# Optimization experiments

Measured on AMD Instinct MI355X. Metric: run time of the kernel, lower is better.

## Reference

```python
import jax, jax.numpy as jnp
import numpy as np


def _conv(x, w, b, pad):
    y = jax.lax.conv_general_dilated(
        x, w, window_strides=(1, 1), padding=[(pad, pad), (pad, pad)],
        dimension_numbers=('NCHW', 'OIHW', 'NCHW'))
    return y + b[None, :, None, None]


def _grid_sample(img, gxn, gyn):
    # img [N,C,H,W]; gxn,gyn [N,H,W] normalized coords.
    # Matches torch grid_sample(mode='bilinear', padding_mode='zeros', align_corners=False).
    N, C, H, W = img.shape
    ix = ((gxn + 1.0) * W - 1.0) * 0.5
    iy = ((gyn + 1.0) * H - 1.0) * 0.5
    ix0 = jnp.floor(ix); iy0 = jnp.floor(iy)
    ix1 = ix0 + 1.0; iy1 = iy0 + 1.0
    wx1 = ix - ix0; wy1 = iy - iy0
    wx0 = 1.0 - wx1; wy0 = 1.0 - wy1
    bidx = jnp.arange(N)[:, None, None]

    def gather(yy, xx):
        valid = (xx >= 0) & (xx < W) & (yy >= 0) & (yy < H)
        xc = jnp.clip(xx, 0, W - 1).astype(jnp.int32)
        yc = jnp.clip(yy, 0, H - 1).astype(jnp.int32)
        v = img[bidx, :, yc, xc]  # [N,H,W,C]
        return jnp.where(valid[..., None], v, jnp.zeros((), img.dtype))

    out = (gather(iy0, ix0) * (wy0 * wx0)[..., None]
           + gather(iy0, ix1) * (wy0 * wx1)[..., None]
           + gather(iy1, ix0) * (wy1 * wx0)[..., None]
           + gather(iy1, ix1) * (wy1 * wx1)[..., None])
    return jnp.transpose(out, (0, 3, 1, 2))  # [N,C,H,W]


def reference(inputs, state, i2h_w, i2h_b, i2f_w, i2f_b, h2f_w, h2f_b,
              flows_w, flows_b, wrap_w, wrap_b):
    B, T, Cin, H, W = inputs.shape
    hid = state.shape[1]
    L = flows_w.shape[0] // 2

    # input-to-hidden for all timesteps at once (as in the torch code)
    i2h = _conv(inputs.reshape(B * T, Cin, H, W), i2h_w, i2h_b, 1)
    i2h = i2h.reshape(B, T, 3 * hid, H, W)
    r_i, u_i, n_i = jnp.split(i2h, 3, axis=2)

    gx, gy = jnp.meshgrid(jnp.arange(W, dtype=inputs.dtype),
                          jnp.arange(H, dtype=inputs.dtype))  # each [H,W]

    def step(h, xs):
        x_t, r_t, u_t, n_t = xs
        f = jnp.tanh(_conv(x_t, i2f_w, i2f_b, 2) + _conv(h, h2f_w, h2f_b, 2))
        flows = _conv(f, flows_w, flows_b, 2).reshape(B, L, 2, H, W)
        # vgrid = grid + (-flow), then normalize by 2*v/size - 1
        vx = gx[None, None] - flows[:, :, 0]
        vy = gy[None, None] - flows[:, :, 1]
        gxn = 2.0 * vx / W - 1.0
        gyn = 2.0 * vy / H - 1.0
        img = jnp.broadcast_to(h[:, None], (B, L, hid, H, W)).reshape(B * L, hid, H, W)
        warped = _grid_sample(img, gxn.reshape(B * L, H, W), gyn.reshape(B * L, H, W))
        warped = warped.reshape(B, L * hid, H, W)
        h2h = _conv(warped, wrap_w, wrap_b, 0)
        r_h, u_h, n_h = jnp.split(h2h, 3, axis=1)
        r = jax.nn.sigmoid(r_t + r_h)
        u = jax.nn.sigmoid(u_t + u_h)
        n = jax.nn.sigmoid(n_t + r * n_h)  # note: sigmoid, faithful to source
        h_new = (1.0 - u) * n + u * h
        return h_new, h_new

    xs = (jnp.swapaxes(inputs, 0, 1),
          jnp.swapaxes(r_i, 0, 1),
          jnp.swapaxes(u_i, 0, 1),
          jnp.swapaxes(n_i, 0, 1))
    h_last, outs = jax.lax.scan(step, state, xs)
    outputs = jnp.swapaxes(outs, 0, 1)  # [B,T,hid,H,W]
    return outputs, h_last


def setup_inputs() -> dict:
    key = jax.random.key(0)
    ks = jax.random.split(key, 8)
    B, T, Cin, H, W = 4, 10, 8, 96, 96
    hid, L = 64, 13

    def w(k, shape):
        fan_in = int(np.prod(shape[1:]))
        return jax.random.normal(k, shape, jnp.float32) * (1.0 / np.sqrt(fan_in))

    return {
        'inputs': jax.random.normal(ks[0], (B, T, Cin, H, W), jnp.float32),
        'state': jnp.zeros((B, hid, H, W), jnp.float32),
        'i2h_w': w(ks[1], (3 * hid, Cin, 3, 3)), 'i2h_b': jnp.zeros((3 * hid,), jnp.float32),
        'i2f_w': w(ks[2], (32, Cin, 5, 5)), 'i2f_b': jnp.zeros((32,), jnp.float32),
        'h2f_w': w(ks[3], (32, hid, 5, 5)), 'h2f_b': jnp.zeros((32,), jnp.float32),
        'flows_w': w(ks[4], (2 * L, 32, 5, 5)), 'flows_b': jnp.zeros((2 * L,), jnp.float32),
        'wrap_w': w(ks[5], (3 * hid, hid * L, 1, 1)), 'wrap_b': jnp.zeros((3 * hid,), jnp.float32),
    }
```

## Files before the change

kernel.cpp:

```cpp
#include <hip/hip_runtime.h>
#include <math.h>

#define HW 9216

typedef __attribute__((ext_vector_type(8))) short short8;
typedef __attribute__((ext_vector_type(4))) short short4v;
typedef __attribute__((ext_vector_type(4))) float float4v;

__device__ __forceinline__ float sigmoidf_(float x) { return 1.0f / (1.0f + expf(-x)); }

__device__ __forceinline__ short bf16rne(float f) {
  unsigned u = __builtin_bit_cast(unsigned, f);
  unsigned r = (u + 0x7FFFu + ((u >> 16) & 1u)) >> 16;
  return (short)r;
}
__device__ __forceinline__ float bf2f(short s) {
  return __builtin_bit_cast(float, ((unsigned)(unsigned short)s) << 16);
}

__global__ __launch_bounds__(256) void k_wconv(const float* __restrict__ w,
                                               short* __restrict__ o)
{
  int i = blockIdx.x * 256 + threadIdx.x;
  if (i >= 192 * 832) return;
  int n = i / 832, k = i % 832;
  int l = k >> 6, c = k & 63;
  o[((size_t)l * 192 + n) * 64 + c] = bf16rne(w[i]);
}

__global__ __launch_bounds__(256) void k_pack(
    const float* __restrict__ wh, const float* __restrict__ wi,
    const float* __restrict__ flw, const float* __restrict__ wih,
    short* __restrict__ whK, short* __restrict__ wiK, short* __restrict__ flK,
    short* __restrict__ i2hK)
{
  int i = blockIdx.x * 256 + threadIdx.x;
  if (i < 51200) {
    int t = i / 2048, rem = i % 2048;
    int o = rem / 64, c = rem % 64;
    whK[i] = bf16rne(wh[((size_t)(o * 64 + c)) * 25 + t]);
  } else if (i < 58368) {
    int j = i - 51200;
    int g = j / 1024, rem = j % 1024;
    int o = rem / 32, k = rem % 32;
    int q = k / 8, ch = k % 8;
    int tap = g * 4 + q;
    wiK[j] = (tap < 25) ? bf16rne(wi[((size_t)(o * 8 + ch)) * 25 + tap]) : (short)0;
  } else if (i < 83968) {
    int j = i - 58368;
    int t = j / 1024, rem = j % 1024;
    int o = rem / 32, c = rem % 32;
    flK[j] = (o < 26) ? bf16rne(flw[((size_t)(o * 32 + c)) * 25 + t]) : (short)0;
  } else {
    int j = i - 83968;
    int g = j / 6144, rem = j % 6144;
    int n = rem / 32, k = rem % 32;
    int q = k / 8, ch = k % 8;
    int tap = g * 4 + q;
    i2hK[j] = (tap < 9) ? bf16rne(wih[((size_t)(n * 8 + ch)) * 9 + tap]) : (short)0;
  }
}

__global__ __launch_bounds__(256) void k_h2bf(const float* __restrict__ st,
                                              short* __restrict__ hbf)
{
  const int tid = threadIdx.x;
  const int pp = tid & 63, cg = tid >> 6;
  const int b = blockIdx.y;
  const int p = blockIdx.x * 64 + pp;
  short s[16];
  #pragma unroll
  for (int k = 0; k < 16; ++k)
    s[k] = bf16rne(st[((size_t)b * 64 + cg * 16 + k) * HW + p]);
  short* dst = hbf + ((size_t)b * HW + p) * 64 + cg * 16;
  *(short8*)dst = *(short8*)&s[0];
  *(short8*)(dst + 8) = *(short8*)&s[8];
}

__global__ __launch_bounds__(256) void k_x2bf(const float* __restrict__ inp,
                                              short* __restrict__ xbf)
{
  const int p  = blockIdx.x * 256 + threadIdx.x;
  const int bt = blockIdx.y;
  short s[8];
  #pragma unroll
  for (int ci = 0; ci < 8; ++ci)
    s[ci] = bf16rne(inp[((size_t)bt * 8 + ci) * HW + p]);
  *(short8*)(xbf + ((size_t)bt * HW + p) * 8) = *(short8*)s;
}

__global__ __launch_bounds__(256) void k_i2h(
    const short* __restrict__ xbf, int t_off,
    const short* __restrict__ wK, const float* __restrict__ bias,
    short* __restrict__ out)
{
  __shared__ __align__(16) short lds_o[192 * 136];
  const int tid  = threadIdx.x;
  const int lane = tid & 63;
  const int w    = tid >> 6;
  const int ml = lane & 15, qd = lane >> 4;
  const int zz = blockIdx.y;
  const int t = (zz >> 2) + t_off, b = zz & 3;
  const int pw0 = blockIdx.x * 128 + w * 32;
  const short* xb = xbf + ((size_t)(b * 10 + t)) * HW * 8;

  short8 afr[2][3];
  #pragma unroll
  for (int s = 0; s < 2; ++s) {
    int px0 = pw0 + s * 16;
    int y0 = px0 / 96, xc0 = px0 % 96;
    #pragma unroll
    for (int g = 0; g < 3; ++g) {
      int tap = g * 4 + qd;
      int dy = tap / 3 - 1;
      int dx = tap % 3 - 1;
      int yy = y0 + dy, xx = xc0 + ml + dx;
      bool v = (tap < 9) && (yy >= 0) && (yy < 96) && (xx >= 0) && (xx < 96);
      short8 a = {};
      if (v) a = *(const short8*)(xb + (size_t)(px0 + ml + dy * 96 + dx) * 8);
      afr[s][g] = a;
    }
  }

  float4v acc[2][12];
  #pragma unroll
  for (int s = 0; s < 2; ++s)
    #pragma unroll
    for (int j = 0; j < 12; ++j)
      #pragma unroll
      for (int r = 0; r < 4; ++r) acc[s][j][r] = 0.0f;

  #pragma unroll
  for (int j = 0; j < 12; ++j) {
    #pragma unroll
    for (int g = 0; g < 3; ++g) {
      short8 bf = *(const short8*)(wK + ((size_t)(g * 192 + j * 16 + ml)) * 32 + qd * 8);
      acc[0][j] = __builtin_amdgcn_mfma_f32_16x16x32_bf16(afr[0][g], bf, acc[0][j], 0, 0, 0);
      acc[1][j] = __builtin_amdgcn_mfma_f32_16x16x32_bf16(afr[1][g], bf, acc[1][j], 0, 0, 0);
    }
  }

  #pragma unroll
  for (int j = 0; j < 12; ++j) {
    float bv = bias[j * 16 + ml];
    #pragma unroll
    for (int s = 0; s < 2; ++s) {
      short4v o4;
      #pragma unroll
      for (int r = 0; r < 4; ++r) o4[r] = bf16rne(acc[s][j][r] + bv);
      *(short4v*)(lds_o + (j * 16 + ml) * 136 + w * 32 + s * 16 + qd * 4) = o4;
    }
  }
  __syncthreads();
  const int pblk = blockIdx.x * 128;
  #pragma unroll
  for (int k = 0; k < 12; ++k) {
    int r = (tid >> 4) + k * 16;
    short8 vvv = *(short8*)(lds_o + r * 136 + (tid & 15) * 8);
    *(short8*)(out + ((size_t)(zz * 192 + r)) * HW + pblk + (tid & 15) * 8) = vvv;
  }
}

__global__ __launch_bounds__(256) void k_f(
    const short* __restrict__ xbf, int t,
    const short* __restrict__ hbf,
    const short* __restrict__ whK,
    const short* __restrict__ wiK,
    const float* __restrict__ bi, const float* __restrict__ bh,
    short* __restrict__ fbf)
{
  const int tid = threadIdx.x;
  const int lane = tid & 63;
  const int w = tid >> 6;
  const int ml = lane & 15, qd = lane >> 4;
  const int b = blockIdx.y;
  const int px0 = blockIdx.x * 64 + w * 16;
  const int y0 = px0 / 96, xc0 = px0 % 96;
  const int xcol = xc0 + ml;
  const int px = px0 + ml;
  const short* hb = hbf + (size_t)b * HW * 64;
  const short* xb = xbf + ((size_t)(b * 10 + t)) * HW * 8;

  float4v acc0 = {0.f, 0.f, 0.f, 0.f};
  float4v acc1 = {0.f, 0.f, 0.f, 0.f};

  #pragma unroll
  for (int ky = 0; ky < 5; ++ky) {
    int yy = y0 + ky - 2;
    if (yy < 0 || yy >= 96) continue;
    #pragma unroll
    for (int kx = 0; kx < 5; ++kx) {
      int xx = xcol + kx - 2;
      bool cv = (xx >= 0) && (xx < 96);
      int off = (ky - 2) * 96 + (kx - 2);
      const short* ap = hb + (size_t)(px + off) * 64 + qd * 8;
      short8 a0 = {}, a1 = {};
      if (cv) { a0 = *(const short8*)ap; a1 = *(const short8*)(ap + 32); }
      int tap = ky * 5 + kx;
      const short* bp = whK + ((size_t)tap * 32 + ml) * 64 + qd * 8;
      short8 b00 = *(const short8*)bp;
      short8 b01 = *(const short8*)(bp + 32);
      short8 b10 = *(const short8*)(bp + 16 * 64);
      short8 b11 = *(const short8*)(bp + 16 * 64 + 32);
      acc0 = __builtin_amdgcn_mfma_f32_16x16x32_bf16(a0, b00, acc0, 0, 0, 0);
      acc0 = __builtin_amdgcn_mfma_f32_16x16x32_bf16(a1, b01, acc0, 0, 0, 0);
      acc1 = __builtin_amdgcn_mfma_f32_16x16x32_bf16(a0, b10, acc1, 0, 0, 0);
      acc1 = __builtin_amdgcn_mfma_f32_16x16x32_bf16(a1, b11, acc1, 0, 0, 0);
    }
  }

  #pragma unroll
  for (int g = 0; g < 7; ++g) {
    int tap = g * 4 + qd;
    int dy = tap / 5 - 2;
    int dx = tap - (dy + 2) * 5 - 2;
    int yy = y0 + dy, xx = xcol + dx;
    bool v = (tap < 25) && (yy >= 0) && (yy < 96) && (xx >= 0) && (xx < 96);
    short8 a = {};
    if (v) a = *(const short8*)(xb + (size_t)(px + dy * 96 + dx) * 8);
    const short* bp = wiK + ((size_t)g * 32 + ml) * 32 + qd * 8;
    short8 b0 = *(const short8*)bp;
    short8 b1 = *(const short8*)(bp + 16 * 32);
    acc0 = __builtin_amdgcn_mfma_f32_16x16x32_bf16(a, b0, acc0, 0, 0, 0);
    acc1 = __builtin_amdgcn_mfma_f32_16x16x32_bf16(a, b1, acc1, 0, 0, 0);
  }

  short* fo = fbf + (size_t)b * HW * 32;
  #pragma unroll
  for (int i = 0; i < 2; ++i) {
    int o = i * 16 + ml;
    float bias = bi[o] + bh[o];
    float4v a = i ? acc1 : acc0;
    #pragma unroll
    for (int r = 0; r < 4; ++r) {
      int p2 = px0 + qd * 4 + r;
      fo[(size_t)p2 * 32 + o] = bf16rne(tanhf(a[r] + bias));
    }
  }
}

__global__ __launch_bounds__(256) void k_flows(
    const short* __restrict__ fbf,
    const short* __restrict__ flK,
    const float* __restrict__ bias,
    float* __restrict__ fls)
{
  const int tid = threadIdx.x;
  const int lane = tid & 63;
  const int w = tid >> 6;
  const int ml = lane & 15, qd = lane >> 4;
  const int b = blockIdx.y;
  const int px0 = blockIdx.x * 64 + w * 16;
  const int y0 = px0 / 96, xc0 = px0 % 96;
  const int xcol = xc0 + ml;
  const int px = px0 + ml;
  const short* fb = fbf + (size_t)b * HW * 32;

  float4v acc0 = {0.f, 0.f, 0.f, 0.f};
  float4v acc1 = {0.f, 0.f, 0.f, 0.f};

  #pragma unroll
  for (int ky = 0; ky < 5; ++ky) {
    int yy = y0 + ky - 2;
    if (yy < 0 || yy >= 96) continue;
    #pragma unroll
    for (int kx = 0; kx < 5; ++kx) {
      int xx = xcol + kx - 2;
      bool cv = (xx >= 0) && (xx < 96);
      int off = (ky - 2) * 96 + (kx - 2);
      short8 a = {};
      if (cv) a = *(const short8*)(fb + (size_t)(px + off) * 32 + qd * 8);
      int tap = ky * 5 + kx;
      const short* bp = flK + ((size_t)tap * 32 + ml) * 32 + qd * 8;
      short8 b0 = *(const short8*)bp;
      short8 b1 = *(const short8*)(bp + 16 * 32);
      acc0 = __builtin_amdgcn_mfma_f32_16x16x32_bf16(a, b0, acc0, 0, 0, 0);
      acc1 = __builtin_amdgcn_mfma_f32_16x16x32_bf16(a, b1, acc1, 0, 0, 0);
    }
  }

  float* fo = fls + (size_t)b * 26 * HW;
  #pragma unroll
  for (int i = 0; i < 2; ++i) {
    int o = i * 16 + ml;
    if (o < 26) {
      float bv = bias[o];
      float4v a = i ? acc1 : acc0;
      #pragma unroll
      for (int r = 0; r < 4; ++r)
        fo[(size_t)o * HW + px0 + qd * 4 + r] = a[r] + bv;
    }
  }
}

__global__ __launch_bounds__(256, 3) void k_fused(
    const float* __restrict__ fls,
    const float* __restrict__ hbase, long long hstr,
    const short* __restrict__ hbf_in,
    const short* __restrict__ i2h,
    const short* __restrict__ wbf,
    const float* __restrict__ wb,
    float* __restrict__ outb, long long ostr,
    short* __restrict__ hbf_out,
    float* __restrict__ lastb)
{
  __shared__ __align__(16) char smem_raw[49920];
  short* lds_w = (short*)smem_raw;
  short* lds_v = lds_w + 192 * 72;
  float* lds_f = (float*)(smem_raw + 36864);
  float* lds_h = (float*)smem_raw;
  short* hpack = (short*)smem_raw;

  const int tid = threadIdx.x;
  const int pp  = tid & 63;
  const int cg  = tid >> 6;
  const int ii  = blockIdx.x;
  const int xcd = ii & 7;
  const int b   = xcd >> 1;
  const int tile = ((ii >> 3) << 1) | (xcd & 1);
  const int p   = tile * 64 + pp;
  const int ypix = p / 96, xpix = p % 96;
  const float* hb  = hbase + (size_t)b * hstr;
  const short* hvp = hbf_in + ((size_t)b * HW) * 64 + cg * 16;
  const float* flb = fls + (size_t)b * 26 * HW;
  const int ml = pp & 15;
  const int qd = pp >> 4;

  #pragma unroll
  for (int it = 0; it < 7; ++it) {
    int idx = it * 256 + tid;
    if (idx < 1664) {
      int c = idx >> 6, pp2 = idx & 63;
      lds_f[pp2 * 26 + c] = flb[(size_t)c * HW + tile * 64 + pp2];
    }
  }

  float4v acc[3][4];
  #pragma unroll
  for (int i = 0; i < 3; ++i)
    #pragma unroll
    for (int j = 0; j < 4; ++j)
      #pragma unroll
      for (int r = 0; r < 4; ++r) acc[i][j][r] = 0.0f;

  int   o_[4];
  float wt_[4];
  short8 u_[4][2];
  short8 wreg[6];
  short vv[16];

  auto comp_offs = [&](int l) {
    float fx = lds_f[pp * 26 + 2 * l];
    float fy = lds_f[pp * 26 + 2 * l + 1];
    float vx = (float)xpix - fx;
    float vy = (float)ypix - fy;
    float gxn = 2.0f * vx / 96.0f - 1.0f;
    float gyn = 2.0f * vy / 96.0f - 1.0f;
    float ix = ((gxn + 1.0f) * 96.0f - 1.0f) * 0.5f;
    float iy = ((gyn + 1.0f) * 96.0f - 1.0f) * 0.5f;
    float x0f = floorf(ix), y0f = floorf(iy);
    float wx1 = ix - x0f, wy1 = iy - y0f;
    float wx0 = 1.0f - wx1, wy0 = 1.0f - wy1;
    int x0 = (int)x0f, y0 = (int)y0f;
    bool vx0 = (x0 >= 0) && (x0 < 96);
    bool vx1 = (x0 + 1 >= 0) && (x0 + 1 < 96);
    bool vy0g = (y0 >= 0) && (y0 < 96);
    bool vy1g = (y0 + 1 >= 0) && (y0 + 1 < 96);
    o_[0] = (vx0 && vy0g) ? (y0 * 96 + x0)           : -1;
    o_[1] = (vx1 && vy0g) ? (y0 * 96 + x0 + 1)       : -1;
    o_[2] = (vx0 && vy1g) ? ((y0 + 1) * 96 + x0)     : -1;
    o_[3] = (vx1 && vy1g) ? ((y0 + 1) * 96 + x0 + 1) : -1;
    wt_[0] = wy0 * wx0; wt_[1] = wy0 * wx1; wt_[2] = wy1 * wx0; wt_[3] = wy1 * wx1;
  };
  auto load_gather = [&]() {
    #pragma unroll
    for (int q = 0; q < 4; ++q) {
      short8 z = {};
      u_[q][0] = z; u_[q][1] = z;
      if (o_[q] >= 0) {
        const short* tp = hvp + (size_t)o_[q] * 64;
        u_[q][0] = *(const short8*)tp;
        u_[q][1] = *(const short8*)(tp + 8);
      }
    }
  };
  auto load_w = [&](int l) {
    const short* wsrc = wbf + (size_t)l * 192 * 64;
    #pragma unroll
    for (int it = 0; it < 6; ++it) {
      int idx = tid + it * 256;
      int n = idx >> 3, c8 = (idx & 7) * 8;
      wreg[it] = *(const short8*)(wsrc + n * 64 + c8);
    }
  };
  auto comp_vv = [&]() {
    float sum[16];
    #pragma unroll
    for (int k = 0; k < 16; ++k) sum[k] = 0.0f;
    #pragma unroll
    for (int q = 0; q < 4; ++q) {
      #pragma unroll
      for (int k = 0; k < 8; ++k) {
        sum[k]     += wt_[q] * bf2f(u_[q][0][k]);
        sum[k + 8] += wt_[q] * bf2f(u_[q][1][k]);
      }
    }
    #pragma unroll
    for (int k = 0; k < 16; ++k) vv[k] = bf16rne(sum[k]);
  };

  __syncthreads();
  load_w(0);
  comp_offs(0);
  load_gather();
  comp_vv();

  for (int l = 0; l < 13; ++l) {
    __syncthreads();
    #pragma unroll
    for (int it = 0; it < 6; ++it) {
      int idx = tid + it * 256;
      int n = idx >> 3, c8 = (idx & 7) * 8;
      *(short8*)(lds_w + n * 72 + c8) = wreg[it];
    }
    *(short8*)(lds_v + pp * 72 + cg * 16)     = *(short8*)&vv[0];
    *(short8*)(lds_v + pp * 72 + cg * 16 + 8) = *(short8*)&vv[8];
    __syncthreads();
    if (l < 12) {
      load_w(l + 1);
      comp_offs(l + 1);
      load_gather();
    }
    #pragma unroll
    for (int ks = 0; ks < 2; ++ks) {
      short8 af[3], bfr[4];
      #pragma unroll
      for (int i = 0; i < 3; ++i)
        af[i] = *(const short8*)(lds_w + (48 * cg + i * 16 + ml) * 72 + ks * 32 + qd * 8);
      #pragma unroll
      for (int j = 0; j < 4; ++j)
        bfr[j] = *(const short8*)(lds_v + (j * 16 + ml) * 72 + ks * 32 + qd * 8);
      #pragma unroll
      for (int i = 0; i < 3; ++i)
        #pragma unroll
        for (int j = 0; j < 4; ++j)
          acc[i][j] = __builtin_amdgcn_mfma_f32_16x16x32_bf16(af[i], bfr[j], acc[i][j], 0, 0, 0);
    }
    if (l < 12) comp_vv();
  }

  __syncthreads();
  #pragma unroll
  for (int i = 0; i < 3; ++i)
    #pragma unroll
    for (int j = 0; j < 4; ++j)
      #pragma unroll
      for (int r = 0; r < 4; ++r) {
        int ch = 48 * cg + i * 16 + qd * 4 + r;
        int px = j * 16 + ml;
        lds_h[ch * 65 + px] = acc[i][j][r];
      }
  __syncthreads();

  const short* i2hb = i2h + (size_t)b * 192 * HW + p;
  float* ob = outb + (size_t)b * ostr;
  float hnv[16];
  #pragma unroll
  for (int k = 0; k < 16; ++k) {
    int cch = cg + k * 4;
    float rh = lds_h[cch * 65 + pp] + wb[cch];
    float uh = lds_h[(64 + cch) * 65 + pp] + wb[64 + cch];
    float nh = lds_h[(128 + cch) * 65 + pp] + wb[128 + cch];
    float rt = bf2f(i2hb[(size_t)cch * HW]);
    float ut = bf2f(i2hb[(size_t)(64 + cch) * HW]);
    float nt = bf2f(i2hb[(size_t)(128 + cch) * HW]);
    float rr = sigmoidf_(rt + rh);
    float uu = sigmoidf_(ut + uh);
    float nn = sigmoidf_(nt + rr * nh);
    float hp = hb[(size_t)cch * HW + p];
    float hn = (1.0f - uu) * nn + uu * hp;
    ob[(size_t)cch * HW + p] = hn;
    if (lastb) lastb[((size_t)b * 64 + cch) * HW + p] = hn;
    hnv[k] = hn;
  }

  __syncthreads();
  #pragma unroll
  for (int k = 0; k < 16; ++k)
    hpack[pp * 80 + cg + 4 * k] = bf16rne(hnv[k]);
  __syncthreads();
  {
    int px = tid >> 2, g = tid & 3;
    short8 a0 = *(short8*)(hpack + px * 80 + g * 16);
    short8 a1 = *(short8*)(hpack + px * 80 + g * 16 + 8);
    short* dst = hbf_out + ((size_t)b * HW + tile * 64 + px) * 64 + g * 16;
    *(short8*)dst = a0;
    *(short8*)(dst + 8) = a1;
  }
}

extern "C" void kernel_launch(void* const* d_in, const int* in_sizes, int n_in,
                              void* d_out, int out_size, void* d_ws, size_t ws_size,
                              hipStream_t stream)
{
  const float* inp   = (const float*)d_in[0];
  const float* state = (const float*)d_in[1];
  const float* i2h_w = (const float*)d_in[2];
  const float* i2h_b = (const float*)d_in[3];
  const float* i2f_w = (const float*)d_in[4];
  const float* i2f_b = (const float*)d_in[5];
  const float* h2f_w = (const float*)d_in[6];
  const float* h2f_b = (const float*)d_in[7];
  const float* fl_w  = (const float*)d_in[8];
  const float* fl_b  = (const float*)d_in[9];
  const float* wr_w  = (const float*)d_in[10];
  const float* wr_b  = (const float*)d_in[11];
  float* out = (float*)d_out;
  float* ws  = (float*)d_ws;

  const long long F_I2HB1 = 3538944;
  const long long F_FBF   = 589824;
  const long long F_FLS   = 958464;
  const long long F_HB    = 1179648;
  const long long F_XBF   = 1474560;
  const long long F_WBF   = 79872;
  const long long F_WHK   = 25600;
  const long long F_WIK   = 3584;
  const long long F_FLK   = 12800;
  const long long F_I2HK  = 9216;
  const long long OB      = (long long)10 * 64 * HW;

  const long long fixed = F_FBF + F_FLS + 2 * F_HB + F_XBF + F_WBF
                        + F_WHK + F_WIK + F_FLK + F_I2HK;
  bool batched = ws_size >= (size_t)(10 * F_I2HB1 + fixed) * 4ULL;
  long long i2h_fl = batched ? 10 * F_I2HB1 : F_I2HB1;

  short* ws_i2h = (short*)ws;
  float* fwp    = ws + i2h_fl;
  float* ws_fbf_f = fwp;              fwp += F_FBF;
  float* ws_fls   = fwp;              fwp += F_FLS;
  float* hbfA_f   = fwp;              fwp += F_HB;
  float* hbfB_f   = fwp;              fwp += F_HB;
  float* xbf_f    = fwp;              fwp += F_XBF;
  float* wbf_f    = fwp;              fwp += F_WBF;
  float* whK_f    = fwp;              fwp += F_WHK;
  float* wiK_f    = fwp;              fwp += F_WIK;
  float* flK_f    = fwp;              fwp += F_FLK;
  float* i2hK_f   = fwp;
  short* ws_fbf  = (short*)ws_fbf_f;
  short* hbfA    = (short*)hbfA_f;
  short* hbfB    = (short*)hbfB_f;
  short* ws_xbf  = (short*)xbf_f;
  short* ws_wbf  = (short*)wbf_f;
  short* ws_whK  = (short*)whK_f;
  short* ws_wiK  = (short*)wiK_f;
  short* ws_flK  = (short*)flK_f;
  short* ws_i2hK = (short*)i2hK_f;

  k_wconv<<<dim3(624), 256, 0, stream>>>(wr_w, ws_wbf);
  k_pack<<<dim3(400), 256, 0, stream>>>(h2f_w, i2f_w, fl_w, i2h_w,
                                        ws_whK, ws_wiK, ws_flK, ws_i2hK);
  k_h2bf<<<dim3(144, 4), 256, 0, stream>>>(state, hbfA);
  k_x2bf<<<dim3(36, 40), 256, 0, stream>>>(inp, ws_xbf);
  if (batched)
    k_i2h<<<dim3(72, 40), 256, 0, stream>>>(ws_xbf, 0, ws_i2hK, i2h_b, ws_i2h);

  for (int t = 0; t < 10; ++t) {
    const float* hbase = (t == 0) ? state : (out + (size_t)(t - 1) * 64 * HW);
    long long hstr = (t == 0) ? (long long)64 * HW : OB;
    short* hin  = (t & 1) ? hbfB : hbfA;
    short* hout = (t & 1) ? hbfA : hbfB;

    if (!batched)
      k_i2h<<<dim3(72, 4), 256, 0, stream>>>(ws_xbf, t, ws_i2hK, i2h_b, ws_i2h);
    k_f<<<dim3(144, 4), 256, 0, stream>>>(ws_xbf, t, hin, ws_whK, ws_wiK,
                                          i2f_b, h2f_b, ws_fbf);
    k_flows<<<dim3(144, 4), 256, 0, stream>>>(ws_fbf, ws_flK, fl_b, ws_fls);

    const short* i2h_t = batched ? (ws_i2h + (size_t)t * 2 * F_I2HB1) : ws_i2h;
    float* outbase = out + (size_t)t * 64 * HW;
    float* lastb = (t == 9) ? (out + (size_t)4 * 10 * 64 * HW) : nullptr;
    k_fused<<<dim3(576), 256, 0, stream>>>(ws_fls, hbase, hstr, hin, i2h_t,
                                           ws_wbf, wr_b, outbase, OB, hout, lastb);
  }
}
```

Baseline: 1.495 ms.

## Load wrap weights straight into registers and double-buffer gathered values in LDS

The fused warp-gather/1x1-conv kernel no longer stages the per-level 192x64 weight slice through LDS. Each thread now loads its MFMA A-fragments directly from global memory into registers. The gathered bilinear values are double-buffered in LDS, which cuts the two barriers per flow level down to one. The grid-coordinate arithmetic is also simplified algebraically. In exchange, each thread issues redundant global weight loads (the slice is read by four lanes, relying on cache), and the weight-load latency now sits right before the next MFMA use.

```diff
diff --git a/kernel.cpp b/kernel.cpp
--- a/kernel.cpp
+++ b/kernel.cpp
@@ -304,12 +304,12 @@
     short* __restrict__ hbf_out,
     float* __restrict__ lastb)
 {
-  __shared__ __align__(16) char smem_raw[49920];
-  short* lds_w = (short*)smem_raw;
-  short* lds_v = lds_w + 192 * 72;
-  float* lds_f = (float*)(smem_raw + 36864);
-  float* lds_h = (float*)smem_raw;
-  short* hpack = (short*)smem_raw;
+  __shared__ __align__(16) char smem_raw[50176];
+  short* lds_v0 = (short*)smem_raw;
+  short* lds_v1 = lds_v0 + 64 * 80;
+  float* lds_f  = (float*)(smem_raw + 20480);
+  float* lds_h  = (float*)smem_raw;
+  short* hpack  = (short*)smem_raw;
 
   const int tid = threadIdx.x;
   const int pp  = tid & 63;
@@ -325,6 +325,7 @@
   const float* flb = fls + (size_t)b * 26 * HW;
   const int ml = pp & 15;
   const int qd = pp >> 4;
+  const short* wfb = wbf + ((size_t)(48 * cg + ml)) * 64 + qd * 8;
 
   #pragma unroll
   for (int it = 0; it < 7; ++it) {
@@ -346,18 +347,14 @@
   int   o_[4];
   float wt_[4];
   short8 u_[4][2];
-  short8 wreg[6];
+  short8 wp[3][2];
   short vv[16];
 
   auto comp_offs = [&](int l) {
     float fx = lds_f[pp * 26 + 2 * l];
     float fy = lds_f[pp * 26 + 2 * l + 1];
-    float vx = (float)xpix - fx;
-    float vy = (float)ypix - fy;
-    float gxn = 2.0f * vx / 96.0f - 1.0f;
-    float gyn = 2.0f * vy / 96.0f - 1.0f;
-    float ix = ((gxn + 1.0f) * 96.0f - 1.0f) * 0.5f;
-    float iy = ((gyn + 1.0f) * 96.0f - 1.0f) * 0.5f;
+    float ix = (float)xpix - fx - 0.5f;
+    float iy = (float)ypix - fy - 0.5f;
     float x0f = floorf(ix), y0f = floorf(iy);
     float wx1 = ix - x0f, wy1 = iy - y0f;
     float wx0 = 1.0f - wx1, wy0 = 1.0f - wy1;
@@ -385,12 +382,11 @@
     }
   };
   auto load_w = [&](int l) {
-    const short* wsrc = wbf + (size_t)l * 192 * 64;
-    #pragma unroll
-    for (int it = 0; it < 6; ++it) {
-      int idx = tid + it * 256;
-      int n = idx >> 3, c8 = (idx & 7) * 8;
-      wreg[it] = *(const short8*)(wsrc + n * 64 + c8);
+    const short* wsrc = wfb + (size_t)l * 192 * 64;
+    #pragma unroll
+    for (int i = 0; i < 3; ++i) {
+      wp[i][0] = *(const short8*)(wsrc + (i * 16) * 64);
+      wp[i][1] = *(const short8*)(wsrc + (i * 16) * 64 + 32);
     }
   };
   auto comp_vv = [&]() {
@@ -408,45 +404,42 @@
     #pragma unroll
     for (int k = 0; k < 16; ++k) vv[k] = bf16rne(sum[k]);
   };
+  auto store_vv = [&](short* buf) {
+    *(short8*)(buf + pp * 80 + cg * 16)     = *(short8*)&vv[0];
+    *(short8*)(buf + pp * 80 + cg * 16 + 8) = *(short8*)&vv[8];
+  };
 
   __syncthreads();
-  load_w(0);
   comp_offs(0);
   load_gather();
+  load_w(0);
   comp_vv();
+  store_vv(lds_v0);
 
   for (int l = 0; l < 13; ++l) {
     __syncthreads();
-    #pragma unroll
-    for (int it = 0; it < 6; ++it) {
-      int idx = tid + it * 256;
-      int n = idx >> 3, c8 = (idx & 7) * 8;
-      *(short8*)(lds_w + n * 72 + c8) = wreg[it];
-    }
-    *(short8*)(lds_v + pp * 72 + cg * 16)     = *(short8*)&vv[0];
-    *(short8*)(lds_v + pp * 72 + cg * 16 + 8) = *(short8*)&vv[8];
-    __syncthreads();
     if (l < 12) {
-      load_w(l + 1);
       comp_offs(l + 1);
       load_gather();
     }
+    short* rbuf = (l & 1) ? lds_v1 : lds_v0;
     #pragma unroll
     for (int ks = 0; ks < 2; ++ks) {
-      short8 af[3], bfr[4];
-      #pragma unroll
-      for (int i = 0; i < 3; ++i)
-        af[i] = *(const short8*)(lds_w + (48 * cg + i * 16 + ml) * 72 + ks * 32 + qd * 8);
+      short8 bfr[4];
       #pragma unroll
       for (int j = 0; j < 4; ++j)
-        bfr[j] = *(const short8*)(lds_v + (j * 16 + ml) * 72 + ks * 32 + qd * 8);
+        bfr[j] = *(const short8*)(rbuf + (j * 16 + ml) * 80 + ks * 32 + qd * 8);
       #pragma unroll
       for (int i = 0; i < 3; ++i)
         #pragma unroll
         for (int j = 0; j < 4; ++j)
-          acc[i][j] = __builtin_amdgcn_mfma_f32_16x16x32_bf16(af[i], bfr[j], acc[i][j], 0, 0, 0);
-    }
-    if (l < 12) comp_vv();
+          acc[i][j] = __builtin_amdgcn_mfma_f32_16x16x32_bf16(wp[i][ks], bfr[j], acc[i][j], 0, 0, 0);
+    }
+    if (l < 12) {
+      load_w(l + 1);
+      comp_vv();
+      store_vv((l & 1) ? lds_v0 : lds_v1);
+    }
   }
 
   __syncthreads();
```

Result: slower. 1.621 ms (+8.5%).
